# Kernel optimization log

Hardware: AMD Instinct MI355X
Metric: run time of the kernel (lower is better)

The kernel has to match this reference:

```python
import jax, jax.numpy as jnp
import numpy as np

B, N, NE = 64, 512, 500
FIELD_DIM, E_DIM, HIDDEN, LATENT = 256, 64, 512, 256


def _lin_init(key, fan_in, fan_out):
    kw, kb = jax.random.split(key)
    s = 1.0 / np.sqrt(fan_in)
    W = jax.random.uniform(kw, (fan_in, fan_out), minval=-s, maxval=s, dtype=jnp.float32)
    b = jax.random.uniform(kb, (fan_out,), minval=-s, maxval=s, dtype=jnp.float32)
    return W, b


def setup_inputs() -> dict:
    key = jax.random.key(0)
    ks = jax.random.split(key, 16)
    inp = {}
    inp['field_atom_lat'] = jax.random.normal(ks[0], (B, N, FIELD_DIM), dtype=jnp.float32)
    inp['mask'] = jax.random.randint(ks[1], (B, N), 0, 2).astype(bool)
    inp['e_feat'] = jax.random.normal(ks[2], (NE, E_DIM), dtype=jnp.float32)
    # query MLP (3 layers): e_dim -> hidden -> hidden -> latent
    inp['q_w1'], inp['q_b1'] = _lin_init(ks[3], E_DIM, HIDDEN)
    inp['q_w2'], inp['q_b2'] = _lin_init(ks[4], HIDDEN, HIDDEN)
    inp['q_w3'], inp['q_b3'] = _lin_init(ks[5], HIDDEN, LATENT)
    # key MLP (3 layers): field_dim -> hidden -> hidden -> latent
    inp['k_w1'], inp['k_b1'] = _lin_init(ks[6], FIELD_DIM, HIDDEN)
    inp['k_w2'], inp['k_b2'] = _lin_init(ks[7], HIDDEN, HIDDEN)
    inp['k_w3'], inp['k_b3'] = _lin_init(ks[8], HIDDEN, LATENT)
    # value MLP (3 layers)
    inp['v_w1'], inp['v_b1'] = _lin_init(ks[9], FIELD_DIM, HIDDEN)
    inp['v_w2'], inp['v_b2'] = _lin_init(ks[10], HIDDEN, HIDDEN)
    inp['v_w3'], inp['v_b3'] = _lin_init(ks[11], HIDDEN, LATENT)
    # out MLP (2 layers): latent -> hidden -> latent
    inp['o_w1'], inp['o_b1'] = _lin_init(ks[12], LATENT, HIDDEN)
    inp['o_w2'], inp['o_b2'] = _lin_init(ks[13], HIDDEN, LATENT)
    return inp


def _mlp3(x, w1, b1, w2, b2, w3, b3):
    h = jax.nn.silu(x @ w1 + b1)
    h = jax.nn.silu(h @ w2 + b2)
    return h @ w3 + b3


def _mlp2(x, w1, b1, w2, b2):
    return jax.nn.silu(x @ w1 + b1) @ w2 + b2


def reference(field_atom_lat, mask, e_feat,
              q_w1, q_b1, q_w2, q_b2, q_w3, q_b3,
              k_w1, k_b1, k_w2, k_b2, k_w3, k_b3,
              v_w1, v_b1, v_w2, v_b2, v_w3, v_b3,
              o_w1, o_b1, o_w2, o_b2):
    latent_dim = q_w3.shape[1]
    scale = latent_dim ** (-0.5)
    q = _mlp3(e_feat, q_w1, q_b1, q_w2, q_b2, q_w3, q_b3)          # [nE, L] (shared across batch)
    k = _mlp3(field_atom_lat, k_w1, k_b1, k_w2, k_b2, k_w3, k_b3)  # [B, N, L]
    v = _mlp3(field_atom_lat, v_w1, v_b1, v_w2, v_b2, v_w3, v_b3)  # [B, N, L]
    scores = jnp.einsum('el,bnl->ben', q, k) * scale               # [B, nE, N]
    scores = jnp.where(mask[:, None, :], scores, jnp.float32(-1e9))
    attn = jax.nn.softmax(scores, axis=2)
    attn = attn * mask[:, None, :].astype(attn.dtype)              # post-softmax mask, as in torch
    out = jnp.einsum('ben,bnl->bel', attn, v)                      # [B, nE, L]
    return _mlp2(out, o_w1, o_b1, o_w2, o_b2)
```

## Files before the change

### kernel.cpp

```cpp
#include <hip/hip_runtime.h>
#include <math.h>

#define BATCH 64
#define N_ATOMS 512
#define NE 500
#define FIELD_DIM 256
#define E_DIM 64
#define HIDDEN 512
#define LATENT 256

typedef short bf16x8 __attribute__((ext_vector_type(8)));
typedef unsigned short u16x8 __attribute__((ext_vector_type(8)));
typedef unsigned short u16x4 __attribute__((ext_vector_type(4)));
typedef float f32x4 __attribute__((ext_vector_type(4)));

__device__ __forceinline__ unsigned short f2bf(float x) {
    unsigned u = __float_as_uint(x);
    unsigned r = (u + 0x7FFFu + ((u >> 16) & 1u)) >> 16;
    return (unsigned short)r;
}
__device__ __forceinline__ float bf2f(unsigned short b) {
    return __uint_as_float(((unsigned)b) << 16);
}
__device__ __forceinline__ float silu_f(float x) { return x / (1.f + __expf(-x)); }

#define GLOAD_LDS16(gptr, lptr)                                                   \
    __builtin_amdgcn_global_load_lds(                                             \
        (const __attribute__((address_space(1))) void*)(gptr),                    \
        (__attribute__((address_space(3))) void*)(lptr), 16, 0, 0)

#define QW1 0
#define QW2 32768
#define QW3 294912
#define KW1 425984
#define KW2 557056
#define KW3 819200
#define VW1 950272
#define VW2 1081344
#define VW3 1343488
#define OW1 1474560
#define OW2 1605632

template <int K, bool SILU>
__device__ __forceinline__ void mlp_layer_ip(
    const unsigned short* __restrict__ Wg, const float* __restrict__ Bg,
    unsigned short* buf, int wave, int lane, int fr, int fq)
{
    const int fb = wave * 64;
    f32x4 acc[4][4];
#pragma unroll
    for (int mf = 0; mf < 4; mf++)
#pragma unroll
        for (int nf = 0; nf < 4; nf++) acc[mf][nf] = (f32x4)0.f;

#pragma unroll
    for (int ks = 0; ks < K / 32; ks++) {
        bf16x8 wf[4], bfr[4];
#pragma unroll
        for (int mf = 0; mf < 4; mf++)
            wf[mf] = *reinterpret_cast<const bf16x8*>(
                Wg + (((long long)(wave * 4 + mf) * (K / 32) + ks) * 64 + lane) * 8);
#pragma unroll
        for (int nf = 0; nf < 4; nf++) {
            int row = nf * 16 + fr;
            bfr[nf] = *reinterpret_cast<const bf16x8*>(
                (const char*)buf + row * (K * 2) +
                ((ks * 64 + fq * 16) ^ ((row & 7) << 4)));
        }
#pragma unroll
        for (int mf = 0; mf < 4; mf++)
#pragma unroll
            for (int nf = 0; nf < 4; nf++)
                acc[mf][nf] = __builtin_amdgcn_mfma_f32_16x16x32_bf16(
                    wf[mf], bfr[nf], acc[mf][nf], 0, 0, 0);
    }
    __syncthreads();

#pragma unroll
    for (int mf = 0; mf < 4; mf++) {
        f32x4 bv = *reinterpret_cast<const f32x4*>(Bg + fb + mf * 16 + fq * 4);
#pragma unroll
        for (int nf = 0; nf < 4; nf++) {
            int row = nf * 16 + fr;
            u16x4 ov;
#pragma unroll
            for (int r = 0; r < 4; r++) {
                float x = acc[mf][nf][r] + bv[r];
                if (SILU) x = silu_f(x);
                ov[r] = f2bf(x);
            }
            *reinterpret_cast<u16x4*>(
                (char*)buf + row * 1024 +
                ((fb * 2 + mf * 32 + fq * 8) ^ ((row & 7) << 4))) = ov;
        }
    }
    __syncthreads();
}

__device__ __forceinline__ void mlp_final512(
    const unsigned short* __restrict__ Wg, const float* __restrict__ Bg,
    const unsigned short* buf, int wave, int lane, int fr, int fq,
    f32x4 (&acc)[2][4])
{
    const int fb = wave * 32;
#pragma unroll
    for (int mf = 0; mf < 2; mf++)
#pragma unroll
        for (int nf = 0; nf < 4; nf++) acc[mf][nf] = (f32x4)0.f;

#pragma unroll
    for (int ks = 0; ks < 16; ks++) {
        bf16x8 wf[2], bfr[4];
#pragma unroll
        for (int mf = 0; mf < 2; mf++)
            wf[mf] = *reinterpret_cast<const bf16x8*>(
                Wg + (((long long)(wave * 2 + mf) * 16 + ks) * 64 + lane) * 8);
#pragma unroll
        for (int nf = 0; nf < 4; nf++) {
            int row = nf * 16 + fr;
            bfr[nf] = *reinterpret_cast<const bf16x8*>(
                (const char*)buf + row * 1024 +
                ((ks * 64 + fq * 16) ^ ((row & 7) << 4)));
        }
#pragma unroll
        for (int mf = 0; mf < 2; mf++)
#pragma unroll
            for (int nf = 0; nf < 4; nf++)
                acc[mf][nf] = __builtin_amdgcn_mfma_f32_16x16x32_bf16(
                    wf[mf], bfr[nf], acc[mf][nf], 0, 0, 0);
    }
#pragma unroll
    for (int mf = 0; mf < 2; mf++) {
        f32x4 bv = *reinterpret_cast<const f32x4*>(Bg + fb + mf * 16 + fq * 4);
#pragma unroll
        for (int nf = 0; nf < 4; nf++)
#pragma unroll
            for (int r = 0; r < 4; r++) acc[mf][nf][r] += bv[r];
    }
}

__global__ __launch_bounds__(512, 2) void fused_qkv(
    const unsigned short* __restrict__ field_bf,
    const unsigned short* __restrict__ efeat_bf,
    const unsigned short* __restrict__ wt,
    const float* __restrict__ qb1, const float* __restrict__ qb2,
    const float* __restrict__ qb3, const float* __restrict__ kb1,
    const float* __restrict__ kb2, const float* __restrict__ kb3,
    const float* __restrict__ vb1, const float* __restrict__ vb2,
    const float* __restrict__ vb3,
    unsigned short* __restrict__ qbuf,
    unsigned short* __restrict__ kbuf,
    unsigned short* __restrict__ vtb)
{
    __shared__ unsigned short buf[64 * 512];
    const int t = threadIdx.x, wave = t >> 6, lane = t & 63;
    const int fr = lane & 15, fq = lane >> 4;
    const int bid = blockIdx.x;

    if (bid < 1024) {
        const int isv = bid >> 9;
        const int m0  = (bid & 511) * 64;
        const unsigned short* W1 = wt + (isv ? VW1 : KW1);
        const unsigned short* W2 = wt + (isv ? VW2 : KW2);
        const unsigned short* W3 = wt + (isv ? VW3 : KW3);
        const float* B1 = isv ? vb1 : kb1;
        const float* B2 = isv ? vb2 : kb2;
        const float* B3 = isv ? vb3 : kb3;

#pragma unroll
        for (int c = wave; c < 32; c += 8) {
            int gi  = c * 64 + lane;
            int row = gi >> 5;
            int g   = gi & 31;
            int gs  = (g & ~7) | ((g & 7) ^ (row & 7));
            GLOAD_LDS16(field_bf + (long long)(m0 + row) * 256 + gs * 8, buf + c * 512);
        }
        __syncthreads();

        mlp_layer_ip<256, true>(W1, B1, buf, wave, lane, fr, fq);
        mlp_layer_ip<512, true>(W2, B2, buf, wave, lane, fr, fq);
        f32x4 acc[2][4];
        mlp_final512(W3, B3, buf, wave, lane, fr, fq, acc);

        if (!isv) {
#pragma unroll
            for (int mf = 0; mf < 2; mf++)
#pragma unroll
                for (int nf = 0; nf < 4; nf++) {
                    int row = m0 + nf * 16 + fr;
                    u16x4 ov;
#pragma unroll
                    for (int r = 0; r < 4; r++) ov[r] = f2bf(acc[mf][nf][r]);
                    *reinterpret_cast<u16x4*>(
                        kbuf + (long long)row * 256 + wave * 32 + mf * 16 + fq * 4) = ov;
                }
        } else {
            __syncthreads();
#pragma unroll
            for (int mf = 0; mf < 2; mf++)
#pragma unroll
                for (int nf = 0; nf < 4; nf++) {
                    int row = nf * 16 + fr;
                    u16x4 ov;
#pragma unroll
                    for (int r = 0; r < 4; r++) ov[r] = f2bf(acc[mf][nf][r]);
                    *reinterpret_cast<u16x4*>(
                        (char*)buf + row * 512 +
                        ((wave * 64 + mf * 32 + fq * 8) ^ ((row & 7) << 4))) = ov;
                }
            __syncthreads();
            int l  = t >> 1;
            int nh = (t & 1) * 32;
            int b  = m0 >> 9, nb = m0 & 511;
            long long base = ((long long)b * 256 + l) * 512 + nb + nh;
#pragma unroll
            for (int q = 0; q < 4; q++) {
                u16x8 ov;
#pragma unroll
                for (int j = 0; j < 8; j++) {
                    int n = nh + q * 8 + j;
                    ov[j] = *reinterpret_cast<const unsigned short*>(
                        (const char*)buf + n * 512 + ((l * 2) ^ ((n & 7) << 4)));
                }
                *reinterpret_cast<u16x8*>(vtb + base + q * 8) = ov;
            }
        }
    } else {
        const int m0 = (bid - 1024) * 64;
        {
            int row = t >> 3;
            int g   = lane & 7;
            int gr  = m0 + row; if (gr >= NE) gr = NE - 1;
            int gs  = g ^ (row & 7);
            GLOAD_LDS16(efeat_bf + (long long)gr * 64 + gs * 8, buf + wave * 512);
        }
        __syncthreads();

        mlp_layer_ip<64, true>(wt + QW1, qb1, buf, wave, lane, fr, fq);
        mlp_layer_ip<512, true>(wt + QW2, qb2, buf, wave, lane, fr, fq);
        f32x4 acc[2][4];
        mlp_final512(wt + QW3, qb3, buf, wave, lane, fr, fq, acc);
#pragma unroll
        for (int mf = 0; mf < 2; mf++)
#pragma unroll
            for (int nf = 0; nf < 4; nf++) {
                int row = m0 + nf * 16 + fr;
                if (row < NE) {
                    u16x4 ov;
#pragma unroll
                    for (int r = 0; r < 4; r++) ov[r] = f2bf(acc[mf][nf][r]);
                    *reinterpret_cast<u16x4*>(
                        qbuf + (long long)row * 256 + wave * 32 + mf * 16 + fq * 4) = ov;
                }
            }
    }
}

__global__ __launch_bounds__(512, 2) void fused_o(
    const unsigned short* __restrict__ X,
    const unsigned short* __restrict__ wt,
    const float* __restrict__ ob1, const float* __restrict__ ob2,
    float* __restrict__ out)
{
    __shared__ unsigned short buf[64 * 512];
    const int t = threadIdx.x, wave = t >> 6, lane = t & 63;
    const int fr = lane & 15, fq = lane >> 4;
    const int m0 = blockIdx.x * 64;

#pragma unroll
    for (int c = wave; c < 32; c += 8) {
        int gi  = c * 64 + lane;
        int row = gi >> 5;
        int g   = gi & 31;
        int gs  = (g & ~7) | ((g & 7) ^ (row & 7));
        GLOAD_LDS16(X + (long long)(m0 + row) * 256 + gs * 8, buf + c * 512);
    }
    __syncthreads();

    mlp_layer_ip<256, true>(wt + OW1, ob1, buf, wave, lane, fr, fq);
    f32x4 acc[2][4];
    mlp_final512(wt + OW2, ob2, buf, wave, lane, fr, fq, acc);

#pragma unroll
    for (int mf = 0; mf < 2; mf++)
#pragma unroll
        for (int nf = 0; nf < 4; nf++) {
            int row = m0 + nf * 16 + fr;
            *reinterpret_cast<f32x4*>(
                out + (long long)row * 256 + wave * 32 + mf * 16 + fq * 4) = acc[mf][nf];
        }
}

__global__ __launch_bounds__(512, 1) void attn_fused(
    const unsigned short* __restrict__ qbuf,
    const unsigned short* __restrict__ kbuf,
    const unsigned short* __restrict__ vt,
    const int* __restrict__ mask,
    unsigned short* __restrict__ attnout)
{
    __shared__ unsigned char LDS[100352];
    unsigned short* Qs = (unsigned short*)LDS;
    unsigned short* Ks = (unsigned short*)(LDS + 32768);
    unsigned short* Ps = (unsigned short*)LDS;
    unsigned short* Vs = (unsigned short*)(LDS + 65536);
    float*          red = (float*)(LDS + 98304);

    const int id = blockIdx.x;
    const int b  = id & 63;
    const int e0 = (id >> 6) * 64;
    const int t = threadIdx.x, wave = t >> 6;
    const int lane = t & 63, fr = lane & 15, fq = lane >> 4;
    const int tr = t >> 3, tg = t & 7;

#pragma unroll
    for (int i = 0; i < 4; i++) {
        int ge = e0 + tr; if (ge >= NE) ge = NE - 1;
        int gi = tg ^ (tr & 7);
        GLOAD_LDS16(qbuf + (long long)ge * 256 + i * 64 + gi * 8,
                    Qs + i * 4096 + wave * 512);
    }
#pragma unroll
    for (int j = 0; j < 8; j++) {
        int n  = j * 64 + tr;
        int gi = tg ^ (n & 7);
        GLOAD_LDS16(kbuf + (long long)(b * 512 + n) * 256 + gi * 8,
                    Ks + j * 4096 + wave * 512);
    }
    int mk[4];
#pragma unroll
    for (int nf = 0; nf < 4; nf++) mk[nf] = mask[b * 512 + wave * 64 + nf * 16 + fr];

    f32x4 acc[4][4];
#pragma unroll
    for (int i = 0; i < 4; i++)
#pragma unroll
        for (int j = 0; j < 4; j++) acc[i][j] = (f32x4)0.f;

    __syncthreads();

    for (int ks = 0; ks < 4; ks++) {
#pragma unroll
        for (int h = 0; h < 2; h++) {
            bf16x8 af[4], bv[4];
#pragma unroll
            for (int mf = 0; mf < 4; mf++) {
                int e = mf * 16 + fr;
                int byo = ks * 8192 + e * 128 + ((h * 64 + fq * 16) ^ ((e & 7) << 4));
                af[mf] = *(const bf16x8*)((const char*)Qs + byo);
            }
#pragma unroll
            for (int nf = 0; nf < 4; nf++) {
                int n = wave * 64 + nf * 16 + fr;
                int byo = n * 128 + ((h * 64 + fq * 16) ^ ((n & 7) << 4));
                bv[nf] = *(const bf16x8*)((const char*)Ks + byo);
            }
#pragma unroll
            for (int mf = 0; mf < 4; mf++)
#pragma unroll
                for (int nf = 0; nf < 4; nf++)
                    acc[mf][nf] = __builtin_amdgcn_mfma_f32_16x16x32_bf16(
                        af[mf], bv[nf], acc[mf][nf], 0, 0, 0);
        }
        if (ks < 3) {
            __syncthreads();
#pragma unroll
            for (int j = 0; j < 8; j++) {
                int n  = j * 64 + tr;
                int gi = tg ^ (n & 7);
                GLOAD_LDS16(kbuf + (long long)(b * 512 + n) * 256 + (ks + 1) * 64 + gi * 8,
                            Ks + j * 4096 + wave * 512);
            }
            __syncthreads();
        }
    }

    const float scale = 0.0625f;
#pragma unroll
    for (int mf = 0; mf < 4; mf++)
#pragma unroll
        for (int nf = 0; nf < 4; nf++)
#pragma unroll
            for (int r = 0; r < 4; r++)
                acc[mf][nf][r] = mk[nf] ? acc[mf][nf][r] * scale : -1e9f;

    float gm[4][4];
#pragma unroll
    for (int mf = 0; mf < 4; mf++)
#pragma unroll
        for (int r = 0; r < 4; r++) {
            float m = fmaxf(fmaxf(acc[mf][0][r], acc[mf][1][r]),
                            fmaxf(acc[mf][2][r], acc[mf][3][r]));
#pragma unroll
            for (int off = 1; off < 16; off <<= 1) m = fmaxf(m, __shfl_xor(m, off, 64));
            if (fr == 0) red[(mf * 16 + fq * 4 + r) * 8 + wave] = m;
        }
    __syncthreads();
#pragma unroll
    for (int mf = 0; mf < 4; mf++)
#pragma unroll
        for (int r = 0; r < 4; r++) {
            int row = mf * 16 + fq * 4 + r;
            float4 a = *(float4*)&red[row * 8];
            float4 c = *(float4*)&red[row * 8 + 4];
            gm[mf][r] = fmaxf(fmaxf(fmaxf(a.x, a.y), fmaxf(a.z, a.w)),
                              fmaxf(fmaxf(c.x, c.y), fmaxf(c.z, c.w)));
        }
    __syncthreads();

    float inv[4][4];
#pragma unroll
    for (int mf = 0; mf < 4; mf++)
#pragma unroll
        for (int r = 0; r < 4; r++) {
            float s = 0.f;
#pragma unroll
            for (int nf = 0; nf < 4; nf++) {
                acc[mf][nf][r] = __expf(acc[mf][nf][r] - gm[mf][r]);
                s += acc[mf][nf][r];
            }
#pragma unroll
            for (int off = 1; off < 16; off <<= 1) s += __shfl_xor(s, off, 64);
            if (fr == 0) red[(mf * 16 + fq * 4 + r) * 8 + wave] = s;
        }
    __syncthreads();
#pragma unroll
    for (int mf = 0; mf < 4; mf++)
#pragma unroll
        for (int r = 0; r < 4; r++) {
            int row = mf * 16 + fq * 4 + r;
            float4 a = *(float4*)&red[row * 8];
            float4 c = *(float4*)&red[row * 8 + 4];
            inv[mf][r] = 1.f / (a.x + a.y + a.z + a.w + c.x + c.y + c.z + c.w);
        }

#pragma unroll
    for (int mf = 0; mf < 4; mf++)
#pragma unroll
        for (int nf = 0; nf < 4; nf++)
#pragma unroll
            for (int r = 0; r < 4; r++) {
                int row = mf * 16 + fq * 4 + r;
                int c   = wave * 64 + nf * 16 + fr;
                float pv = mk[nf] ? acc[mf][nf][r] * inv[mf][r] : 0.f;
                *(unsigned short*)((char*)Ps + row * 1024 + ((c * 2) ^ ((row & 7) << 4))) =
                    f2bf(pv);
            }
    __syncthreads();

    f32x4 acc2[4][2];
#pragma unroll
    for (int i = 0; i < 4; i++)
#pragma unroll
        for (int j = 0; j < 2; j++) acc2[i][j] = (f32x4)0.f;

#pragma unroll
    for (int j = 0; j < 4; j++) {
        int l  = j * 64 + tr;
        int gi = tg ^ (l & 7);
        GLOAD_LDS16(vt + (long long)(b * 256 + l) * 512 + gi * 8,
                    Vs + j * 4096 + wave * 512);
    }
    __syncthreads();

    for (int ks = 0; ks < 8; ks++) {
#pragma unroll
        for (int h = 0; h < 2; h++) {
            bf16x8 af[4], bv[2];
#pragma unroll
            for (int mf = 0; mf < 4; mf++) {
                int e = mf * 16 + fr;
                int byo = e * 1024 + ((ks * 128 + h * 64 + fq * 16) ^ ((e & 7) << 4));
                af[mf] = *(const bf16x8*)((const char*)Ps + byo);
            }
#pragma unroll
            for (int nf = 0; nf < 2; nf++) {
                int l = wave * 32 + nf * 16 + fr;
                int byo = l * 128 + ((h * 64 + fq * 16) ^ ((l & 7) << 4));
                bv[nf] = *(const bf16x8*)((const char*)Vs + byo);
            }
#pragma unroll
            for (int mf = 0; mf < 4; mf++)
#pragma unroll
                for (int nf = 0; nf < 2; nf++)
                    acc2[mf][nf] = __builtin_amdgcn_mfma_f32_16x16x32_bf16(
                        af[mf], bv[nf], acc2[mf][nf], 0, 0, 0);
        }
        if (ks < 7) {
            __syncthreads();
#pragma unroll
            for (int j = 0; j < 4; j++) {
                int l  = j * 64 + tr;
                int gi = tg ^ (l & 7);
                GLOAD_LDS16(vt + (long long)(b * 256 + l) * 512 + (ks + 1) * 64 + gi * 8,
                            Vs + j * 4096 + wave * 512);
            }
            __syncthreads();
        }
    }

#pragma unroll
    for (int mf = 0; mf < 4; mf++)
#pragma unroll
        for (int nf = 0; nf < 2; nf++)
#pragma unroll
            for (int r = 0; r < 4; r++) {
                int e = e0 + mf * 16 + fq * 4 + r;
                if (e < NE) {
                    int l = wave * 32 + nf * 16 + fr;
                    attnout[((long long)b * NE + e) * 256 + l] = f2bf(acc2[mf][nf][r]);
                }
            }
}

__global__ __launch_bounds__(256) void f32_to_bf16(
    const float* __restrict__ in, unsigned short* __restrict__ out, long long n8)
{
    long long i      = (long long)blockIdx.x * 256 + threadIdx.x;
    long long stride = (long long)gridDim.x * 256;
    for (; i < n8; i += stride) {
        const float4* p = reinterpret_cast<const float4*>(in + i * 8);
        float4 a = p[0], b = p[1];
        u16x8 o;
        o[0] = f2bf(a.x); o[1] = f2bf(a.y); o[2] = f2bf(a.z); o[3] = f2bf(a.w);
        o[4] = f2bf(b.x); o[5] = f2bf(b.y); o[6] = f2bf(b.z); o[7] = f2bf(b.w);
        *reinterpret_cast<u16x8*>(out + i * 8) = o;
    }
}

__global__ __launch_bounds__(256) void wt_pack(
    const float* w0, const float* w1, const float* w2, const float* w3,
    const float* w4, const float* w5, const float* w6, const float* w7,
    const float* w8, const float* w9, const float* w10, unsigned short* dst)
{
    const int Kd[11] = {64, 512, 512, 256, 512, 512, 256, 512, 512, 256, 512};
    const int Nd[11] = {512, 512, 256, 512, 512, 256, 512, 512, 256, 512, 256};
    const long long Od[11] = {QW1, QW2, QW3, KW1, KW2, KW3, VW1, VW2, VW3, OW1, OW2};
    const int z = blockIdx.z;
    const float* src = z == 0 ? w0 : z == 1 ? w1 : z == 2 ? w2 : z == 3 ? w3 :
                       z == 4 ? w4 : z == 5 ? w5 : z == 6 ? w6 : z == 7 ? w7 :
                       z == 8 ? w8 : z == 9 ? w9 : w10;
    const int K = Kd[z], N = Nd[z];
    const int k0 = blockIdx.y * 64, n0 = blockIdx.x * 64;
    if (k0 >= K || n0 >= N) return;

    __shared__ float tf[64][65];
    const int t = threadIdx.x;
    {
        const int r = t >> 2;
        const int c0 = (t & 3) * 16;
        const float* srow = src + (long long)(k0 + r) * N + n0 + c0;
#pragma unroll
        for (int q = 0; q < 4; q++) {
            float4 xv = *reinterpret_cast<const float4*>(srow + q * 4);
            tf[r][c0 + q * 4 + 0] = xv.x;
            tf[r][c0 + q * 4 + 1] = xv.y;
            tf[r][c0 + q * 4 + 2] = xv.z;
            tf[r][c0 + q * 4 + 3] = xv.w;
        }
    }
    __syncthreads();

#pragma unroll
    for (int it = 0; it < 2; it++) {
        int wi = t + it * 256;
        int nc = wi & 63;
        int k8 = wi >> 6;
        int kg = k0 + k8 * 8;
        int ks = kg >> 5;
        int fq = (kg >> 3) & 3;
        int f16 = (n0 + nc) >> 4;
        int fr  = nc & 15;
        u16x8 ov;
#pragma unroll
        for (int e = 0; e < 8; e++) ov[e] = f2bf(tf[k8 * 8 + e][nc]);
        long long off = Od[z] +
            (((long long)f16 * (K / 32) + ks) * 64 + fq * 16 + fr) * 8;
        *reinterpret_cast<u16x8*>(dst + off) = ov;
    }
}

extern "C" void kernel_launch(void* const* d_in, const int* in_sizes, int n_in,
                              void* d_out, int out_size, void* d_ws, size_t ws_size,
                              hipStream_t stream)
{
    const float* field = (const float*)d_in[0];
    const int*   mask  = (const int*)d_in[1];
    const float* efeat = (const float*)d_in[2];
    const float* q_w1 = (const float*)d_in[3];  const float* q_b1 = (const float*)d_in[4];
    const float* q_w2 = (const float*)d_in[5];  const float* q_b2 = (const float*)d_in[6];
    const float* q_w3 = (const float*)d_in[7];  const float* q_b3 = (const float*)d_in[8];
    const float* k_w1 = (const float*)d_in[9];  const float* k_b1 = (const float*)d_in[10];
    const float* k_w2 = (const float*)d_in[11]; const float* k_b2 = (const float*)d_in[12];
    const float* k_w3 = (const float*)d_in[13]; const float* k_b3 = (const float*)d_in[14];
    const float* v_w1 = (const float*)d_in[15]; const float* v_b1 = (const float*)d_in[16];
    const float* v_w2 = (const float*)d_in[17]; const float* v_b2 = (const float*)d_in[18];
    const float* v_w3 = (const float*)d_in[19]; const float* v_b3 = (const float*)d_in[20];
    const float* o_w1 = (const float*)d_in[21]; const float* o_b1 = (const float*)d_in[22];
    const float* o_w2 = (const float*)d_in[23]; const float* o_b2 = (const float*)d_in[24];

    unsigned short* ws = (unsigned short*)d_ws;
    unsigned short* field_bf = ws;
    unsigned short* efeat_bf = ws + 8388608;
    unsigned short* wt       = ws + 8420608;
    unsigned short* qbuf     = ws + 10157312;
    unsigned short* kbuf     = ws + 10285312;
    unsigned short* vtb      = ws + 18673920;
    unsigned short* attnout  = ws + 27062528;

    f32_to_bf16<<<dim3(2048), dim3(256), 0, stream>>>(field, field_bf, 1048576);
    f32_to_bf16<<<dim3(16),   dim3(256), 0, stream>>>(efeat, efeat_bf, 4000);
    wt_pack<<<dim3(8, 8, 11), dim3(256), 0, stream>>>(
        q_w1, q_w2, q_w3, k_w1, k_w2, k_w3, v_w1, v_w2, v_w3, o_w1, o_w2, wt);

    fused_qkv<<<dim3(1032), dim3(512), 0, stream>>>(
        field_bf, efeat_bf, wt, q_b1, q_b2, q_b3, k_b1, k_b2, k_b3,
        v_b1, v_b2, v_b3, qbuf, kbuf, vtb);

    attn_fused<<<dim3(512), dim3(512), 0, stream>>>(qbuf, kbuf, vtb, mask, attnout);

    fused_o<<<dim3(500), dim3(512), 0, stream>>>(
        attnout, wt, o_b1, o_b2, (float*)d_out);
}
```

Measured before the change: 240.4 us.

## Use 128-row tiles with 16 waves per block in MLP kernels

The fused QKV and output MLP kernels now process 128 rows per block with 1024 threads (16 waves) instead of 64 rows with 512 threads. Each wave owns fewer output features but more rows, so each weight fragment loaded from global memory is reused across twice as many rows. Weight fragments are also prefetched one k-step ahead. The cost is double the LDS per block, one block per CU, half as many blocks (fewer waves to spread across CUs), and higher register pressure from 16 accumulators per wave.

```diff
diff --git a/kernel.cpp b/kernel.cpp
--- a/kernel.cpp
+++ b/kernel.cpp
@@ -42,45 +42,56 @@
 #define OW2 1605632
 
 template <int K, bool SILU>
-__device__ __forceinline__ void mlp_layer_ip(
+__device__ __forceinline__ void mlp_layer_w16(
     const unsigned short* __restrict__ Wg, const float* __restrict__ Bg,
     unsigned short* buf, int wave, int lane, int fr, int fq)
 {
-    const int fb = wave * 64;
-    f32x4 acc[4][4];
-#pragma unroll
-    for (int mf = 0; mf < 4; mf++)
-#pragma unroll
-        for (int nf = 0; nf < 4; nf++) acc[mf][nf] = (f32x4)0.f;
-
-#pragma unroll
-    for (int ks = 0; ks < K / 32; ks++) {
-        bf16x8 wf[4], bfr[4];
-#pragma unroll
-        for (int mf = 0; mf < 4; mf++)
-            wf[mf] = *reinterpret_cast<const bf16x8*>(
-                Wg + (((long long)(wave * 4 + mf) * (K / 32) + ks) * 64 + lane) * 8);
-#pragma unroll
-        for (int nf = 0; nf < 4; nf++) {
+    constexpr int NS = K / 32;
+    const int fb = wave * 32;
+    const unsigned short* w0 = Wg + (long long)(wave * 2 + 0) * NS * 512 + lane * 8;
+    const unsigned short* w1 = Wg + (long long)(wave * 2 + 1) * NS * 512 + lane * 8;
+
+    f32x4 acc[2][8];
+#pragma unroll
+    for (int mf = 0; mf < 2; mf++)
+#pragma unroll
+        for (int nf = 0; nf < 8; nf++) acc[mf][nf] = (f32x4)0.f;
+
+    bf16x8 wfA0 = *reinterpret_cast<const bf16x8*>(w0);
+    bf16x8 wfA1 = *reinterpret_cast<const bf16x8*>(w1);
+
+#pragma unroll
+    for (int ks = 0; ks < NS; ks++) {
+        bf16x8 wfB0, wfB1;
+        if (ks + 1 < NS) {
+            wfB0 = *reinterpret_cast<const bf16x8*>(w0 + (ks + 1) * 512);
+            wfB1 = *reinterpret_cast<const bf16x8*>(w1 + (ks + 1) * 512);
+        }
+        bf16x8 bfr[8];
+#pragma unroll
+        for (int nf = 0; nf < 8; nf++) {
             int row = nf * 16 + fr;
             bfr[nf] = *reinterpret_cast<const bf16x8*>(
                 (const char*)buf + row * (K * 2) +
                 ((ks * 64 + fq * 16) ^ ((row & 7) << 4)));
         }
 #pragma unroll
-        for (int mf = 0; mf < 4; mf++)
-#pragma unroll
-            for (int nf = 0; nf < 4; nf++)
-                acc[mf][nf] = __builtin_amdgcn_mfma_f32_16x16x32_bf16(
-                    wf[mf], bfr[nf], acc[mf][nf], 0, 0, 0);
-    }
-    __syncthreads();
-
-#pragma unroll
-    for (int mf = 0; mf < 4; mf++) {
+        for (int nf = 0; nf < 8; nf++)
+            acc[0][nf] = __builtin_amdgcn_mfma_f32_16x16x32_bf16(
+                wfA0, bfr[nf], acc[0][nf], 0, 0, 0);
+#pragma unroll
+        for (int nf = 0; nf < 8; nf++)
+            acc[1][nf] = __builtin_amdgcn_mfma_f32_16x16x32_bf16(
+                wfA1, bfr[nf], acc[1][nf], 0, 0, 0);
+        if (ks + 1 < NS) { wfA0 = wfB0; wfA1 = wfB1; }
+    }
+    __syncthreads();
+
+#pragma unroll
+    for (int mf = 0; mf < 2; mf++) {
         f32x4 bv = *reinterpret_cast<const f32x4*>(Bg + fb + mf * 16 + fq * 4);
 #pragma unroll
-        for (int nf = 0; nf < 4; nf++) {
+        for (int nf = 0; nf < 8; nf++) {
             int row = nf * 16 + fr;
             u16x4 ov;
 #pragma unroll
@@ -97,49 +108,60 @@
     __syncthreads();
 }
 
-__device__ __forceinline__ void mlp_final512(
+__device__ __forceinline__ void mlp_final_w16(
     const unsigned short* __restrict__ Wg, const float* __restrict__ Bg,
     const unsigned short* buf, int wave, int lane, int fr, int fq,
-    f32x4 (&acc)[2][4])
-{
-    const int fb = wave * 32;
-#pragma unroll
-    for (int mf = 0; mf < 2; mf++)
-#pragma unroll
-        for (int nf = 0; nf < 4; nf++) acc[mf][nf] = (f32x4)0.f;
-
+    f32x4 (&acc)[8])
+{
+    const unsigned short* w0 = Wg + (long long)wave * 16 * 512 + lane * 8;
+#pragma unroll
+    for (int nf = 0; nf < 8; nf++) acc[nf] = (f32x4)0.f;
+
+    bf16x8 wfA = *reinterpret_cast<const bf16x8*>(w0);
 #pragma unroll
     for (int ks = 0; ks < 16; ks++) {
-        bf16x8 wf[2], bfr[4];
-#pragma unroll
-        for (int mf = 0; mf < 2; mf++)
-            wf[mf] = *reinterpret_cast<const bf16x8*>(
-                Wg + (((long long)(wave * 2 + mf) * 16 + ks) * 64 + lane) * 8);
-#pragma unroll
-        for (int nf = 0; nf < 4; nf++) {
+        bf16x8 wfB;
+        if (ks + 1 < 16) wfB = *reinterpret_cast<const bf16x8*>(w0 + (ks + 1) * 512);
+        bf16x8 bfr[8];
+#pragma unroll
+        for (int nf = 0; nf < 8; nf++) {
             int row = nf * 16 + fr;
             bfr[nf] = *reinterpret_cast<const bf16x8*>(
                 (const char*)buf + row * 1024 +
                 ((ks * 64 + fq * 16) ^ ((row & 7) << 4)));
         }
 #pragma unroll
-        for (int mf = 0; mf < 2; mf++)
-#pragma unroll
-            for (int nf = 0; nf < 4; nf++)
-                acc[mf][nf] = __builtin_amdgcn_mfma_f32_16x16x32_bf16(
-                    wf[mf], bfr[nf], acc[mf][nf], 0, 0, 0);
-    }
-#pragma unroll
-    for (int mf = 0; mf < 2; mf++) {
-        f32x4 bv = *reinterpret_cast<const f32x4*>(Bg + fb + mf * 16 + fq * 4);
-#pragma unroll
-        for (int nf = 0; nf < 4; nf++)
-#pragma unroll
-            for (int r = 0; r < 4; r++) acc[mf][nf][r] += bv[r];
-    }
-}
-
-__global__ __launch_bounds__(512, 2) void fused_qkv(
+        for (int nf = 0; nf < 8; nf++)
+            acc[nf] = __builtin_amdgcn_mfma_f32_16x16x32_bf16(
+                wfA, bfr[nf], acc[nf], 0, 0, 0);
+        if (ks + 1 < 16) wfA = wfB;
+    }
+    f32x4 bv = *reinterpret_cast<const f32x4*>(Bg + wave * 16 + fq * 4);
+#pragma unroll
+    for (int nf = 0; nf < 8; nf++)
+#pragma unroll
+        for (int r = 0; r < 4; r++) acc[nf][r] += bv[r];
+}
+
+template <int K>
+__device__ __forceinline__ void stage_tile(
+    const unsigned short* __restrict__ X, long long Mmax, long long m0,
+    unsigned short* buf, int wave, int lane)
+{
+    constexpr int GPL = K / 8;
+    constexpr int NCH = 128 * GPL / 64;
+#pragma unroll
+    for (int c = wave; c < NCH; c += 16) {
+        int gi  = c * 64 + lane;
+        int row = gi / GPL;
+        int g   = gi % GPL;
+        long long gr = m0 + row; if (gr >= Mmax) gr = Mmax - 1;
+        int gs  = (g & ~7) | ((g & 7) ^ (row & 7));
+        GLOAD_LDS16(X + gr * K + gs * 8, buf + c * 512);
+    }
+}
+
+__global__ __launch_bounds__(1024, 1) void fused_qkv(
     const unsigned short* __restrict__ field_bf,
     const unsigned short* __restrict__ efeat_bf,
     const unsigned short* __restrict__ wt,
@@ -152,14 +174,14 @@
     unsigned short* __restrict__ kbuf,
     unsigned short* __restrict__ vtb)
 {
-    __shared__ unsigned short buf[64 * 512];
+    __shared__ unsigned short buf[128 * 512];
     const int t = threadIdx.x, wave = t >> 6, lane = t & 63;
     const int fr = lane & 15, fq = lane >> 4;
     const int bid = blockIdx.x;
 
-    if (bid < 1024) {
-        const int isv = bid >> 9;
-        const int m0  = (bid & 511) * 64;
+    if (bid < 512) {
+        const int isv = bid >> 8;
+        const long long m0 = (long long)(bid & 255) * 128;
         const unsigned short* W1 = wt + (isv ? VW1 : KW1);
         const unsigned short* W2 = wt + (isv ? VW2 : KW2);
         const unsigned short* W3 = wt + (isv ? VW3 : KW3);
@@ -167,52 +189,42 @@
         const float* B2 = isv ? vb2 : kb2;
         const float* B3 = isv ? vb3 : kb3;
 
-#pragma unroll
-        for (int c = wave; c < 32; c += 8) {
-            int gi  = c * 64 + lane;
-            int row = gi >> 5;
-            int g   = gi & 31;
-            int gs  = (g & ~7) | ((g & 7) ^ (row & 7));
-            GLOAD_LDS16(field_bf + (long long)(m0 + row) * 256 + gs * 8, buf + c * 512);
-        }
+        stage_tile<256>(field_bf, 32768, m0, buf, wave, lane);
         __syncthreads();
 
-        mlp_layer_ip<256, true>(W1, B1, buf, wave, lane, fr, fq);
-        mlp_layer_ip<512, true>(W2, B2, buf, wave, lane, fr, fq);
-        f32x4 acc[2][4];
-        mlp_final512(W3, B3, buf, wave, lane, fr, fq, acc);
+        mlp_layer_w16<256, true>(W1, B1, buf, wave, lane, fr, fq);
+        mlp_layer_w16<512, true>(W2, B2, buf, wave, lane, fr, fq);
+        f32x4 acc[8];
+        mlp_final_w16(W3, B3, buf, wave, lane, fr, fq, acc);
 
         if (!isv) {
 #pragma unroll
-            for (int mf = 0; mf < 2; mf++)
-#pragma unroll
-                for (int nf = 0; nf < 4; nf++) {
-                    int row = m0 + nf * 16 + fr;
-                    u16x4 ov;
-#pragma unroll
-                    for (int r = 0; r < 4; r++) ov[r] = f2bf(acc[mf][nf][r]);
-                    *reinterpret_cast<u16x4*>(
-                        kbuf + (long long)row * 256 + wave * 32 + mf * 16 + fq * 4) = ov;
-                }
+            for (int nf = 0; nf < 8; nf++) {
+                long long row = m0 + nf * 16 + fr;
+                u16x4 ov;
+#pragma unroll
+                for (int r = 0; r < 4; r++) ov[r] = f2bf(acc[nf][r]);
+                *reinterpret_cast<u16x4*>(
+                    kbuf + row * 256 + wave * 16 + fq * 4) = ov;
+            }
         } else {
             __syncthreads();
 #pragma unroll
-            for (int mf = 0; mf < 2; mf++)
-#pragma unroll
-                for (int nf = 0; nf < 4; nf++) {
-                    int row = nf * 16 + fr;
-                    u16x4 ov;
-#pragma unroll
-                    for (int r = 0; r < 4; r++) ov[r] = f2bf(acc[mf][nf][r]);
-                    *reinterpret_cast<u16x4*>(
-                        (char*)buf + row * 512 +
-                        ((wave * 64 + mf * 32 + fq * 8) ^ ((row & 7) << 4))) = ov;
-                }
+            for (int nf = 0; nf < 8; nf++) {
+                int row = nf * 16 + fr;
+                u16x4 ov;
+#pragma unroll
+                for (int r = 0; r < 4; r++) ov[r] = f2bf(acc[nf][r]);
+                *reinterpret_cast<u16x4*>(
+                    (char*)buf + row * 512 +
+                    ((wave * 32 + fq * 8) ^ ((row & 7) << 4))) = ov;
+            }
             __syncthreads();
-            int l  = t >> 1;
-            int nh = (t & 1) * 32;
-            int b  = m0 >> 9, nb = m0 & 511;
-            long long base = ((long long)b * 256 + l) * 512 + nb + nh;
+            int l  = t >> 2;
+            int nh = (t & 3) * 32;
+            long long b  = m0 >> 9;
+            int nb = (int)(m0 & 511);
+            long long base = (b * 256 + l) * 512 + nb + nh;
 #pragma unroll
             for (int q = 0; q < 4; q++) {
                 u16x8 ov;
@@ -226,69 +238,52 @@
             }
         }
     } else {
-        const int m0 = (bid - 1024) * 64;
-        {
-            int row = t >> 3;
-            int g   = lane & 7;
-            int gr  = m0 + row; if (gr >= NE) gr = NE - 1;
-            int gs  = g ^ (row & 7);
-            GLOAD_LDS16(efeat_bf + (long long)gr * 64 + gs * 8, buf + wave * 512);
-        }
+        const long long m0 = (long long)(bid - 512) * 128;
+        stage_tile<64>(efeat_bf, NE, m0, buf, wave, lane);
         __syncthreads();
 
-        mlp_layer_ip<64, true>(wt + QW1, qb1, buf, wave, lane, fr, fq);
-        mlp_layer_ip<512, true>(wt + QW2, qb2, buf, wave, lane, fr, fq);
-        f32x4 acc[2][4];
-        mlp_final512(wt + QW3, qb3, buf, wave, lane, fr, fq, acc);
-#pragma unroll
-        for (int mf = 0; mf < 2; mf++)
-#pragma unroll
-            for (int nf = 0; nf < 4; nf++) {
-                int row = m0 + nf * 16 + fr;
-                if (row < NE) {
-                    u16x4 ov;
-#pragma unroll
-                    for (int r = 0; r < 4; r++) ov[r] = f2bf(acc[mf][nf][r]);
-                    *reinterpret_cast<u16x4*>(
-                        qbuf + (long long)row * 256 + wave * 32 + mf * 16 + fq * 4) = ov;
-                }
-            }
-    }
-}
-
-__global__ __launch_bounds__(512, 2) void fused_o(
+        mlp_layer_w16<64, true>(wt + QW1, qb1, buf, wave, lane, fr, fq);
+        mlp_layer_w16<512, true>(wt + QW2, qb2, buf, wave, lane, fr, fq);
+        f32x4 acc[8];
+        mlp_final_w16(wt + QW3, qb3, buf, wave, lane, fr, fq, acc);
+#pragma unroll
+        for (int nf = 0; nf < 8; nf++) {
+            long long row = m0 + nf * 16 + fr;
+            if (row < NE) {
+                u16x4 ov;
+#pragma unroll
+                for (int r = 0; r < 4; r++) ov[r] = f2bf(acc[nf][r]);
+                *reinterpret_cast<u16x4*>(
+                    qbuf + row * 256 + wave * 16 + fq * 4) = ov;
+            }
+        }
+    }
+}
+
+__global__ __launch_bounds__(1024, 1) void fused_o(
     const unsigned short* __restrict__ X,
     const unsigned short* __restrict__ wt,
     const float* __restrict__ ob1, const float* __restrict__ ob2,
     float* __restrict__ out)
 {
-    __shared__ unsigned short buf[64 * 512];
+    __shared__ unsigned short buf[128 * 512];
     const int t = threadIdx.x, wave = t >> 6, lane = t & 63;
     const int fr = lane & 15, fq = lane >> 4;
-    const int m0 = blockIdx.x * 64;
-
-#pragma unroll
-    for (int c = wave; c < 32; c += 8) {
-        int gi  = c * 64 + lane;
-        int row = gi >> 5;
-        int g   = gi & 31;
-        int gs  = (g & ~7) | ((g & 7) ^ (row & 7));
-        GLOAD_LDS16(X + (long long)(m0 + row) * 256 + gs * 8, buf + c * 512);
-    }
-    __syncthreads();
-
-    mlp_layer_ip<256, true>(wt + OW1, ob1, buf, wave, lane, fr, fq);
-    f32x4 acc[2][4];
-    mlp_final512(wt + OW2, ob2, buf, wave, lane, fr, fq, acc);
-
-#pragma unroll
-    for (int mf = 0; mf < 2; mf++)
-#pragma unroll
-        for (int nf = 0; nf < 4; nf++) {
-            int row = m0 + nf * 16 + fr;
-            *reinterpret_cast<f32x4*>(
-                out + (long long)row * 256 + wave * 32 + mf * 16 + fq * 4) = acc[mf][nf];
-        }
+    const long long m0 = (long long)blockIdx.x * 128;
+
+    stage_tile<256>(X, 32000, m0, buf, wave, lane);
+    __syncthreads();
+
+    mlp_layer_w16<256, true>(wt + OW1, ob1, buf, wave, lane, fr, fq);
+    f32x4 acc[8];
+    mlp_final_w16(wt + OW2, ob2, buf, wave, lane, fr, fq, acc);
+
+#pragma unroll
+    for (int nf = 0; nf < 8; nf++) {
+        long long row = m0 + nf * 16 + fr;
+        *reinterpret_cast<f32x4*>(
+            out + row * 256 + wave * 16 + fq * 4) = acc[nf];
+    }
 }
 
 __global__ __launch_bounds__(512, 1) void attn_fused(
@@ -612,12 +607,12 @@
     wt_pack<<<dim3(8, 8, 11), dim3(256), 0, stream>>>(
         q_w1, q_w2, q_w3, k_w1, k_w2, k_w3, v_w1, v_w2, v_w3, o_w1, o_w2, wt);
 
-    fused_qkv<<<dim3(1032), dim3(512), 0, stream>>>(
+    fused_qkv<<<dim3(516), dim3(1024), 0, stream>>>(
         field_bf, efeat_bf, wt, q_b1, q_b2, q_b3, k_b1, k_b2, k_b3,
         v_b1, v_b2, v_b3, qbuf, kbuf, vtb);
 
     attn_fused<<<dim3(512), dim3(512), 0, stream>>>(qbuf, kbuf, vtb, mask, attnout);
 
-    fused_o<<<dim3(500), dim3(512), 0, stream>>>(
+    fused_o<<<dim3(250), dim3(1024), 0, stream>>>(
         attnout, wt, o_b1, o_b2, (float*)d_out);
 }
```

Measured after the change: 257.4 us. 1.07x slower.

## Process 128 rows per block in MLP kernels to reuse weight fragments

Applied to the files above, without the earlier changes.

The QKV and output MLP kernels now handle two 64-row tiles per block, held in a doubled LDS buffer. Each weight fragment loaded from global memory feeds MFMAs for both tiles, halving weight traffic per row. Grid sizes are halved to match. This doubles LDS use to 128KB and doubles the accumulator registers, which may cut occupancy and leave fewer blocks to fill the GPU.

```diff
diff --git a/kernel.cpp b/kernel.cpp
--- a/kernel.cpp
+++ b/kernel.cpp
@@ -41,38 +41,48 @@
 #define OW1 1474560
 #define OW2 1605632
 
+#define HALF_U 32768
+#define HALF_B 65536
+
 template <int K, bool SILU>
-__device__ __forceinline__ void mlp_layer_ip(
+__device__ __forceinline__ void mlp_layer_dual(
     const unsigned short* __restrict__ Wg, const float* __restrict__ Bg,
     unsigned short* buf, int wave, int lane, int fr, int fq)
 {
+    constexpr int NS = K / 32;
     const int fb = wave * 64;
-    f32x4 acc[4][4];
-#pragma unroll
-    for (int mf = 0; mf < 4; mf++)
-#pragma unroll
-        for (int nf = 0; nf < 4; nf++) acc[mf][nf] = (f32x4)0.f;
-
-#pragma unroll
-    for (int ks = 0; ks < K / 32; ks++) {
-        bf16x8 wf[4], bfr[4];
+    f32x4 acc[2][4][4];
+#pragma unroll
+    for (int t = 0; t < 2; t++)
+#pragma unroll
+        for (int mf = 0; mf < 4; mf++)
+#pragma unroll
+            for (int nf = 0; nf < 4; nf++) acc[t][mf][nf] = (f32x4)0.f;
+
+#pragma unroll
+    for (int ks = 0; ks < NS; ks++) {
+        bf16x8 wf[4];
 #pragma unroll
         for (int mf = 0; mf < 4; mf++)
             wf[mf] = *reinterpret_cast<const bf16x8*>(
-                Wg + (((long long)(wave * 4 + mf) * (K / 32) + ks) * 64 + lane) * 8);
+                Wg + (((long long)(wave * 4 + mf) * NS + ks) * 64 + lane) * 8);
+        bf16x8 b0[4], b1[4];
 #pragma unroll
         for (int nf = 0; nf < 4; nf++) {
             int row = nf * 16 + fr;
-            bfr[nf] = *reinterpret_cast<const bf16x8*>(
-                (const char*)buf + row * (K * 2) +
-                ((ks * 64 + fq * 16) ^ ((row & 7) << 4)));
+            int off = row * (K * 2) + ((ks * 64 + fq * 16) ^ ((row & 7) << 4));
+            b0[nf] = *reinterpret_cast<const bf16x8*>((const char*)buf + off);
+            b1[nf] = *reinterpret_cast<const bf16x8*>((const char*)buf + HALF_B + off);
         }
 #pragma unroll
         for (int mf = 0; mf < 4; mf++)
 #pragma unroll
-            for (int nf = 0; nf < 4; nf++)
-                acc[mf][nf] = __builtin_amdgcn_mfma_f32_16x16x32_bf16(
-                    wf[mf], bfr[nf], acc[mf][nf], 0, 0, 0);
+            for (int nf = 0; nf < 4; nf++) {
+                acc[0][mf][nf] = __builtin_amdgcn_mfma_f32_16x16x32_bf16(
+                    wf[mf], b0[nf], acc[0][mf][nf], 0, 0, 0);
+                acc[1][mf][nf] = __builtin_amdgcn_mfma_f32_16x16x32_bf16(
+                    wf[mf], b1[nf], acc[1][mf][nf], 0, 0, 0);
+            }
     }
     __syncthreads();
 
@@ -80,62 +90,90 @@
     for (int mf = 0; mf < 4; mf++) {
         f32x4 bv = *reinterpret_cast<const f32x4*>(Bg + fb + mf * 16 + fq * 4);
 #pragma unroll
-        for (int nf = 0; nf < 4; nf++) {
-            int row = nf * 16 + fr;
-            u16x4 ov;
-#pragma unroll
-            for (int r = 0; r < 4; r++) {
-                float x = acc[mf][nf][r] + bv[r];
-                if (SILU) x = silu_f(x);
-                ov[r] = f2bf(x);
-            }
-            *reinterpret_cast<u16x4*>(
-                (char*)buf + row * 1024 +
-                ((fb * 2 + mf * 32 + fq * 8) ^ ((row & 7) << 4))) = ov;
-        }
-    }
-    __syncthreads();
-}
-
-__device__ __forceinline__ void mlp_final512(
+        for (int t = 0; t < 2; t++)
+#pragma unroll
+            for (int nf = 0; nf < 4; nf++) {
+                int row = nf * 16 + fr;
+                u16x4 ov;
+#pragma unroll
+                for (int r = 0; r < 4; r++) {
+                    float x = acc[t][mf][nf][r] + bv[r];
+                    if (SILU) x = silu_f(x);
+                    ov[r] = f2bf(x);
+                }
+                *reinterpret_cast<u16x4*>(
+                    (char*)buf + t * HALF_B + row * 1024 +
+                    ((fb * 2 + mf * 32 + fq * 8) ^ ((row & 7) << 4))) = ov;
+            }
+    }
+    __syncthreads();
+}
+
+__device__ __forceinline__ void mlp_final_dual(
     const unsigned short* __restrict__ Wg, const float* __restrict__ Bg,
     const unsigned short* buf, int wave, int lane, int fr, int fq,
-    f32x4 (&acc)[2][4])
+    f32x4 (&acc)[2][2][4])
 {
     const int fb = wave * 32;
 #pragma unroll
-    for (int mf = 0; mf < 2; mf++)
-#pragma unroll
-        for (int nf = 0; nf < 4; nf++) acc[mf][nf] = (f32x4)0.f;
+    for (int t = 0; t < 2; t++)
+#pragma unroll
+        for (int mf = 0; mf < 2; mf++)
+#pragma unroll
+            for (int nf = 0; nf < 4; nf++) acc[t][mf][nf] = (f32x4)0.f;
 
 #pragma unroll
     for (int ks = 0; ks < 16; ks++) {
-        bf16x8 wf[2], bfr[4];
+        bf16x8 wf[2];
 #pragma unroll
         for (int mf = 0; mf < 2; mf++)
             wf[mf] = *reinterpret_cast<const bf16x8*>(
                 Wg + (((long long)(wave * 2 + mf) * 16 + ks) * 64 + lane) * 8);
+        bf16x8 b0[4], b1[4];
 #pragma unroll
         for (int nf = 0; nf < 4; nf++) {
             int row = nf * 16 + fr;
-            bfr[nf] = *reinterpret_cast<const bf16x8*>(
-                (const char*)buf + row * 1024 +
-                ((ks * 64 + fq * 16) ^ ((row & 7) << 4)));
+            int off = row * 1024 + ((ks * 64 + fq * 16) ^ ((row & 7) << 4));
+            b0[nf] = *reinterpret_cast<const bf16x8*>((const char*)buf + off);
+            b1[nf] = *reinterpret_cast<const bf16x8*>((const char*)buf + HALF_B + off);
         }
 #pragma unroll
         for (int mf = 0; mf < 2; mf++)
 #pragma unroll
-            for (int nf = 0; nf < 4; nf++)
-                acc[mf][nf] = __builtin_amdgcn_mfma_f32_16x16x32_bf16(
-                    wf[mf], bfr[nf], acc[mf][nf], 0, 0, 0);
+            for (int nf = 0; nf < 4; nf++) {
+                acc[0][mf][nf] = __builtin_amdgcn_mfma_f32_16x16x32_bf16(
+                    wf[mf], b0[nf], acc[0][mf][nf], 0, 0, 0);
+                acc[1][mf][nf] = __builtin_amdgcn_mfma_f32_16x16x32_bf16(
+                    wf[mf], b1[nf], acc[1][mf][nf], 0, 0, 0);
+            }
     }
 #pragma unroll
     for (int mf = 0; mf < 2; mf++) {
         f32x4 bv = *reinterpret_cast<const f32x4*>(Bg + fb + mf * 16 + fq * 4);
 #pragma unroll
-        for (int nf = 0; nf < 4; nf++)
-#pragma unroll
-            for (int r = 0; r < 4; r++) acc[mf][nf][r] += bv[r];
+        for (int t = 0; t < 2; t++)
+#pragma unroll
+            for (int nf = 0; nf < 4; nf++)
+#pragma unroll
+                for (int r = 0; r < 4; r++) acc[t][mf][nf][r] += bv[r];
+    }
+}
+
+template <int K>
+__device__ __forceinline__ void stage64(
+    const unsigned short* __restrict__ X, long long Mmax, long long m0,
+    unsigned short* half, int wave, int lane)
+{
+    constexpr int GPL = K / 8;
+    constexpr int NCH = 64 * GPL / 64;
+#pragma unroll
+    for (int c = wave; c < NCH; c += 8) {
+        int gi  = c * 64 + lane;
+        int row = gi / GPL;
+        int g   = gi % GPL;
+        long long gr = m0 + row; if (gr >= Mmax) gr = Mmax - 1;
+        int gs  = (g & ~7) | ((g & 7) ^ (row & 7));
+        GLOAD_LDS16(X + gr * K + gs * 8, half + c * 512);
     }
 }
 
@@ -152,14 +190,14 @@
     unsigned short* __restrict__ kbuf,
     unsigned short* __restrict__ vtb)
 {
-    __shared__ unsigned short buf[64 * 512];
+    __shared__ unsigned short buf[2 * HALF_U];
     const int t = threadIdx.x, wave = t >> 6, lane = t & 63;
     const int fr = lane & 15, fq = lane >> 4;
     const int bid = blockIdx.x;
 
-    if (bid < 1024) {
-        const int isv = bid >> 9;
-        const int m0  = (bid & 511) * 64;
+    if (bid < 512) {
+        const int isv = bid >> 8;
+        const long long m0 = (long long)(bid & 255) * 128;
         const unsigned short* W1 = wt + (isv ? VW1 : KW1);
         const unsigned short* W2 = wt + (isv ? VW2 : KW2);
         const unsigned short* W3 = wt + (isv ? VW3 : KW3);
@@ -167,92 +205,92 @@
         const float* B2 = isv ? vb2 : kb2;
         const float* B3 = isv ? vb3 : kb3;
 
-#pragma unroll
-        for (int c = wave; c < 32; c += 8) {
-            int gi  = c * 64 + lane;
-            int row = gi >> 5;
-            int g   = gi & 31;
-            int gs  = (g & ~7) | ((g & 7) ^ (row & 7));
-            GLOAD_LDS16(field_bf + (long long)(m0 + row) * 256 + gs * 8, buf + c * 512);
-        }
+        stage64<256>(field_bf, 32768, m0,      buf,          wave, lane);
+        stage64<256>(field_bf, 32768, m0 + 64, buf + HALF_U, wave, lane);
         __syncthreads();
 
-        mlp_layer_ip<256, true>(W1, B1, buf, wave, lane, fr, fq);
-        mlp_layer_ip<512, true>(W2, B2, buf, wave, lane, fr, fq);
-        f32x4 acc[2][4];
-        mlp_final512(W3, B3, buf, wave, lane, fr, fq, acc);
+        mlp_layer_dual<256, true>(W1, B1, buf, wave, lane, fr, fq);
+        mlp_layer_dual<512, true>(W2, B2, buf, wave, lane, fr, fq);
+        f32x4 acc[2][2][4];
+        mlp_final_dual(W3, B3, buf, wave, lane, fr, fq, acc);
 
         if (!isv) {
 #pragma unroll
-            for (int mf = 0; mf < 2; mf++)
-#pragma unroll
-                for (int nf = 0; nf < 4; nf++) {
-                    int row = m0 + nf * 16 + fr;
-                    u16x4 ov;
-#pragma unroll
-                    for (int r = 0; r < 4; r++) ov[r] = f2bf(acc[mf][nf][r]);
-                    *reinterpret_cast<u16x4*>(
-                        kbuf + (long long)row * 256 + wave * 32 + mf * 16 + fq * 4) = ov;
-                }
+            for (int tt = 0; tt < 2; tt++)
+#pragma unroll
+                for (int mf = 0; mf < 2; mf++)
+#pragma unroll
+                    for (int nf = 0; nf < 4; nf++) {
+                        long long row = m0 + tt * 64 + nf * 16 + fr;
+                        u16x4 ov;
+#pragma unroll
+                        for (int r = 0; r < 4; r++) ov[r] = f2bf(acc[tt][mf][nf][r]);
+                        *reinterpret_cast<u16x4*>(
+                            kbuf + row * 256 + wave * 32 + mf * 16 + fq * 4) = ov;
+                    }
         } else {
             __syncthreads();
 #pragma unroll
-            for (int mf = 0; mf < 2; mf++)
-#pragma unroll
-                for (int nf = 0; nf < 4; nf++) {
-                    int row = nf * 16 + fr;
-                    u16x4 ov;
-#pragma unroll
-                    for (int r = 0; r < 4; r++) ov[r] = f2bf(acc[mf][nf][r]);
-                    *reinterpret_cast<u16x4*>(
-                        (char*)buf + row * 512 +
-                        ((wave * 64 + mf * 32 + fq * 8) ^ ((row & 7) << 4))) = ov;
-                }
+            for (int tt = 0; tt < 2; tt++)
+#pragma unroll
+                for (int mf = 0; mf < 2; mf++)
+#pragma unroll
+                    for (int nf = 0; nf < 4; nf++) {
+                        int row = nf * 16 + fr;
+                        u16x4 ov;
+#pragma unroll
+                        for (int r = 0; r < 4; r++) ov[r] = f2bf(acc[tt][mf][nf][r]);
+                        *reinterpret_cast<u16x4*>(
+                            (char*)buf + tt * HALF_B + row * 512 +
+                            ((wave * 64 + mf * 32 + fq * 8) ^ ((row & 7) << 4))) = ov;
+                    }
             __syncthreads();
             int l  = t >> 1;
             int nh = (t & 1) * 32;
-            int b  = m0 >> 9, nb = m0 & 511;
-            long long base = ((long long)b * 256 + l) * 512 + nb + nh;
-#pragma unroll
-            for (int q = 0; q < 4; q++) {
-                u16x8 ov;
-#pragma unroll
-                for (int j = 0; j < 8; j++) {
-                    int n = nh + q * 8 + j;
-                    ov[j] = *reinterpret_cast<const unsigned short*>(
-                        (const char*)buf + n * 512 + ((l * 2) ^ ((n & 7) << 4)));
+            long long b  = m0 >> 9;
+#pragma unroll
+            for (int tt = 0; tt < 2; tt++) {
+                int nb = (int)((m0 + tt * 64) & 511);
+                long long base = (b * 256 + l) * 512 + nb + nh;
+#pragma unroll
+                for (int q = 0; q < 4; q++) {
+                    u16x8 ov;
+#pragma unroll
+                    for (int j = 0; j < 8; j++) {
+                        int n = nh + q * 8 + j;
+                        ov[j] = *reinterpret_cast<const unsigned short*>(
+                            (const char*)buf + tt * HALF_B + n * 512 +
+                            ((l * 2) ^ ((n & 7) << 4)));
+                    }
+                    *reinterpret_cast<u16x8*>(vtb + base + q * 8) = ov;
                 }
-                *reinterpret_cast<u16x8*>(vtb + base + q * 8) = ov;
             }
         }
     } else {
-        const int m0 = (bid - 1024) * 64;
-        {
-            int row = t >> 3;
-            int g   = lane & 7;
-            int gr  = m0 + row; if (gr >= NE) gr = NE - 1;
-            int gs  = g ^ (row & 7);
-            GLOAD_LDS16(efeat_bf + (long long)gr * 64 + gs * 8, buf + wave * 512);
-        }
+        const long long m0 = (long long)(bid - 512) * 128;
+        stage64<64>(efeat_bf, NE, m0,      buf,          wave, lane);
+        stage64<64>(efeat_bf, NE, m0 + 64, buf + HALF_U, wave, lane);
         __syncthreads();
 
-        mlp_layer_ip<64, true>(wt + QW1, qb1, buf, wave, lane, fr, fq);
-        mlp_layer_ip<512, true>(wt + QW2, qb2, buf, wave, lane, fr, fq);
-        f32x4 acc[2][4];
-        mlp_final512(wt + QW3, qb3, buf, wave, lane, fr, fq, acc);
-#pragma unroll
-        for (int mf = 0; mf < 2; mf++)
-#pragma unroll
-            for (int nf = 0; nf < 4; nf++) {
-                int row = m0 + nf * 16 + fr;
-                if (row < NE) {
-                    u16x4 ov;
-#pragma unroll
-                    for (int r = 0; r < 4; r++) ov[r] = f2bf(acc[mf][nf][r]);
-                    *reinterpret_cast<u16x4*>(
-                        qbuf + (long long)row * 256 + wave * 32 + mf * 16 + fq * 4) = ov;
+        mlp_layer_dual<64, true>(wt + QW1, qb1, buf, wave, lane, fr, fq);
+        mlp_layer_dual<512, true>(wt + QW2, qb2, buf, wave, lane, fr, fq);
+        f32x4 acc[2][2][4];
+        mlp_final_dual(wt + QW3, qb3, buf, wave, lane, fr, fq, acc);
+#pragma unroll
+        for (int tt = 0; tt < 2; tt++)
+#pragma unroll
+            for (int mf = 0; mf < 2; mf++)
+#pragma unroll
+                for (int nf = 0; nf < 4; nf++) {
+                    long long row = m0 + tt * 64 + nf * 16 + fr;
+                    if (row < NE) {
+                        u16x4 ov;
+#pragma unroll
+                        for (int r = 0; r < 4; r++) ov[r] = f2bf(acc[tt][mf][nf][r]);
+                        *reinterpret_cast<u16x4*>(
+                            qbuf + row * 256 + wave * 32 + mf * 16 + fq * 4) = ov;
+                    }
                 }
-            }
     }
 }
 
@@ -262,33 +300,29 @@
     const float* __restrict__ ob1, const float* __restrict__ ob2,
     float* __restrict__ out)
 {
-    __shared__ unsigned short buf[64 * 512];
+    __shared__ unsigned short buf[2 * HALF_U];
     const int t = threadIdx.x, wave = t >> 6, lane = t & 63;
     const int fr = lane & 15, fq = lane >> 4;
-    const int m0 = blockIdx.x * 64;
-
-#pragma unroll
-    for (int c = wave; c < 32; c += 8) {
-        int gi  = c * 64 + lane;
-        int row = gi >> 5;
-        int g   = gi & 31;
-        int gs  = (g & ~7) | ((g & 7) ^ (row & 7));
-        GLOAD_LDS16(X + (long long)(m0 + row) * 256 + gs * 8, buf + c * 512);
-    }
-    __syncthreads();
-
-    mlp_layer_ip<256, true>(wt + OW1, ob1, buf, wave, lane, fr, fq);
-    f32x4 acc[2][4];
-    mlp_final512(wt + OW2, ob2, buf, wave, lane, fr, fq, acc);
-
-#pragma unroll
-    for (int mf = 0; mf < 2; mf++)
-#pragma unroll
-        for (int nf = 0; nf < 4; nf++) {
-            int row = m0 + nf * 16 + fr;
-            *reinterpret_cast<f32x4*>(
-                out + (long long)row * 256 + wave * 32 + mf * 16 + fq * 4) = acc[mf][nf];
-        }
+    const long long m0 = (long long)blockIdx.x * 128;
+
+    stage64<256>(X, 32000, m0,      buf,          wave, lane);
+    stage64<256>(X, 32000, m0 + 64, buf + HALF_U, wave, lane);
+    __syncthreads();
+
+    mlp_layer_dual<256, true>(wt + OW1, ob1, buf, wave, lane, fr, fq);
+    f32x4 acc[2][2][4];
+    mlp_final_dual(wt + OW2, ob2, buf, wave, lane, fr, fq, acc);
+
+#pragma unroll
+    for (int tt = 0; tt < 2; tt++)
+#pragma unroll
+        for (int mf = 0; mf < 2; mf++)
+#pragma unroll
+            for (int nf = 0; nf < 4; nf++) {
+                long long row = m0 + tt * 64 + nf * 16 + fr;
+                *reinterpret_cast<f32x4*>(
+                    out + row * 256 + wave * 32 + mf * 16 + fq * 4) = acc[tt][mf][nf];
+            }
 }
 
 __global__ __launch_bounds__(512, 1) void attn_fused(
@@ -612,12 +646,12 @@
     wt_pack<<<dim3(8, 8, 11), dim3(256), 0, stream>>>(
         q_w1, q_w2, q_w3, k_w1, k_w2, k_w3, v_w1, v_w2, v_w3, o_w1, o_w2, wt);
 
-    fused_qkv<<<dim3(1032), dim3(512), 0, stream>>>(
+    fused_qkv<<<dim3(516), dim3(512), 0, stream>>>(
         field_bf, efeat_bf, wt, q_b1, q_b2, q_b3, k_b1, k_b2, k_b3,
         v_b1, v_b2, v_b3, qbuf, kbuf, vtb);
 
     attn_fused<<<dim3(512), dim3(512), 0, stream>>>(qbuf, kbuf, vtb, mask, attnout);
 
-    fused_o<<<dim3(500), dim3(512), 0, stream>>>(
+    fused_o<<<dim3(250), dim3(512), 0, stream>>>(
         attnout, wt, o_b1, o_b2, (float*)d_out);
 }
```

New measurement: 265.9 us. +10.6%, slower.
